# Optimization experiments

Measured on AMD Instinct MI355X. Metric: run time of the kernel, lower is better.

Reference implementation:

```python
import jax, jax.numpy as jnp
import numpy as np

B, S, D, H = 8, 1024, 512, 8
HD = D // H
EPS = 1e-5


def layer_norm(x, g, b):
    m = jnp.mean(x, axis=-1, keepdims=True)
    v = jnp.mean(jnp.square(x - m), axis=-1, keepdims=True)
    return (x - m) * jax.lax.rsqrt(v + EPS) * g + b


def mha(x, w_in, b_in, w_out, b_out):
    # x: [B,S,D]; w_in: [3D,D]; PyTorch MultiheadAttention math (no dropout, eval)
    b, s, d = x.shape
    qkv = x @ w_in.T + b_in                      # [B,S,3D]
    q, k, v = jnp.split(qkv, 3, axis=-1)
    q = q.reshape(b, s, H, HD)
    k = k.reshape(b, s, H, HD)
    v = v.reshape(b, s, H, HD)
    scores = jnp.einsum('bqhd,bkhd->bhqk', q, k) / np.sqrt(HD)
    a = jax.nn.softmax(scores, axis=-1)
    o = jnp.einsum('bhqk,bkhd->bqhd', a, v).reshape(b, s, d)
    return o @ w_out.T + b_out


def interp_linear(y, out_size):
    # y: [B,S_in,D]; torch F.interpolate(mode='linear', align_corners=False)
    s_in = y.shape[1]
    scale = s_in / out_size
    src = (jnp.arange(out_size, dtype=jnp.float32) + 0.5) * scale - 0.5
    src = jnp.clip(src, 0.0, s_in - 1.0)
    i0 = jnp.floor(src).astype(jnp.int32)
    i1 = jnp.minimum(i0 + 1, s_in - 1)
    w = (src - i0.astype(jnp.float32))[None, :, None]
    return y[:, i0, :] * (1.0 - w) + y[:, i1, :] * w


def setup_inputs() -> dict:
    key = jax.random.key(0)
    ks = jax.random.split(key, 16)
    sd = 0.02
    return {
        'x': jax.random.normal(ks[0], (B, S, D), jnp.float32),
        'w_in1': jax.random.normal(ks[1], (3 * D, D), jnp.float32) * sd,
        'b_in1': jnp.zeros((3 * D,), jnp.float32),
        'w_out1': jax.random.normal(ks[2], (D, D), jnp.float32) * sd,
        'b_out1': jnp.zeros((D,), jnp.float32),
        'w_in2': jax.random.normal(ks[3], (3 * D, D), jnp.float32) * sd,
        'b_in2': jnp.zeros((3 * D,), jnp.float32),
        'w_out2': jax.random.normal(ks[4], (D, D), jnp.float32) * sd,
        'b_out2': jnp.zeros((D,), jnp.float32),
        'g1': jnp.ones((D,), jnp.float32), 'beta1': jnp.zeros((D,), jnp.float32),
        'g2': jnp.ones((D,), jnp.float32), 'beta2': jnp.zeros((D,), jnp.float32),
        'g3': jnp.ones((D,), jnp.float32), 'beta3': jnp.zeros((D,), jnp.float32),
        'w_ff1': jax.random.normal(ks[5], (4 * D, D), jnp.float32) * sd,
        'b_ff1': jnp.zeros((4 * D,), jnp.float32),
        'w_ff2': jax.random.normal(ks[6], (D, 4 * D), jnp.float32) * sd,
        'b_ff2': jnp.zeros((D,), jnp.float32),
    }


def reference(x, w_in1, b_in1, w_out1, b_out1, w_in2, b_in2, w_out2, b_out2,
              g1, beta1, g2, beta2, g3, beta3, w_ff1, b_ff1, w_ff2, b_ff2):
    a1 = mha(x, w_in1, b_in1, w_out1, b_out1)
    x = layer_norm(x + a1, g1, beta1)
    # avg_pool1d kernel=2 stride=2 ceil_mode (S even -> exact halving)
    pooled = x.reshape(B, S // 2, 2, D).mean(axis=2)
    a2 = mha(pooled, w_in2, b_in2, w_out2, b_out2)
    up = interp_linear(a2, S)
    x = layer_norm(x + up, g2, beta2)
    h = jax.nn.gelu(x @ w_ff1.T + b_ff1, approximate=False)
    ff = h @ w_ff2.T + b_ff2
    return layer_norm(x + ff, g3, beta3)
```

## Files before the change

### kernel.cpp

```cpp
#include <hip/hip_runtime.h>
#include <hip/hip_bf16.h>
#include <math.h>

typedef __hip_bfloat16 bf16;
typedef __attribute__((ext_vector_type(8))) short short8;
typedef __attribute__((ext_vector_type(4))) short s4v;
typedef __attribute__((ext_vector_type(4))) float f32x4;

__device__ __forceinline__ float ldf(const float* p, size_t i) { return p[i]; }
__device__ __forceinline__ float ldf(const bf16*  p, size_t i) { return __bfloat162float(p[i]); }
__device__ __forceinline__ void  stf(float* p, size_t i, float v) { p[i] = v; }
__device__ __forceinline__ void  stf(bf16*  p, size_t i, float v) { p[i] = __float2bfloat16(v); }

__device__ __forceinline__ float ex2(float x) { return __builtin_amdgcn_exp2f(x); }

__device__ __forceinline__ void gl16(const void* gp, void* lp) {
    __builtin_amdgcn_global_load_lds(
        (const __attribute__((address_space(1))) void*)gp,
        (__attribute__((address_space(3))) void*)lp, 16, 0, 0);
}

__global__ __launch_bounds__(256) void cvt_kernel(
    const float* __restrict__ src, bf16* __restrict__ dst, int n)
{
    for (int i = blockIdx.x * 256 + threadIdx.x; i < n; i += gridDim.x * 256)
        dst[i] = __float2bfloat16(src[i]);
}

__global__ __launch_bounds__(256) void cvt_w(
    const float* __restrict__ s0, const float* __restrict__ s1,
    const float* __restrict__ s2, const float* __restrict__ s3,
    const float* __restrict__ s4, const float* __restrict__ s5,
    bf16* __restrict__ dst)
{
    int i = blockIdx.x * 256 + threadIdx.x;
    const float* s; int off;
    if      (i <  786432) { s = s0; off = 0; }
    else if (i < 1048576) { s = s1; off =  786432; }
    else if (i < 1835008) { s = s2; off = 1048576; }
    else if (i < 2097152) { s = s3; off = 1835008; }
    else if (i < 3145728) { s = s4; off = 2097152; }
    else                  { s = s5; off = 3145728; }
    dst[i] = __float2bfloat16(s[i - off]);
}

template <int EPI>
__global__ __launch_bounds__(256) void gemm_mfma(
    const bf16* __restrict__ A, const bf16* __restrict__ W,
    const float* __restrict__ bias, bf16* __restrict__ C,
    int M, int N, int K)
{
    __shared__ __align__(16) bf16 Asl[128 * 64];
    __shared__ __align__(16) bf16 Bsl[128 * 64];

    const int tid  = threadIdx.x;
    const int lane = tid & 63;
    const int wave = tid >> 6;
    const int wm   = wave >> 1;
    const int wn   = wave & 1;
    const int l15  = lane & 15;
    const int quad = lane >> 4;
    const int sr   = lane >> 3;
    const int sc   = (lane & 7) * 8;

    const int row0 = blockIdx.y * 128, col0 = blockIdx.x * 128;

    f32x4 acc[4][4] = {};

    for (int k0 = 0; k0 < K; k0 += 64) {
        __syncthreads();
        #pragma unroll
        for (int t = 0; t < 4; t++) {
            int r0 = wave * 32 + t * 8;
            int r  = r0 + sr;
            gl16(&A[(size_t)(row0 + r) * K + k0 + sc], &Asl[r0 * 64]);
            gl16(&W[(size_t)(col0 + r) * K + k0 + sc], &Bsl[r0 * 64]);
        }
        __syncthreads();

        #pragma unroll
        for (int ks = 0; ks < 64; ks += 32) {
            short8 af[4], bfr[4];
            #pragma unroll
            for (int mt = 0; mt < 4; mt++)
                af[mt] = *(const short8*)&Asl[(wm * 64 + mt * 16 + l15) * 64 + ks + quad * 8];
            #pragma unroll
            for (int nt = 0; nt < 4; nt++)
                bfr[nt] = *(const short8*)&Bsl[(wn * 64 + nt * 16 + l15) * 64 + ks + quad * 8];
            #pragma unroll
            for (int mt = 0; mt < 4; mt++)
                #pragma unroll
                for (int nt = 0; nt < 4; nt++)
                    acc[mt][nt] = __builtin_amdgcn_mfma_f32_16x16x32_bf16(
                        af[mt], bfr[nt], acc[mt][nt], 0, 0, 0);
        }
    }

    #pragma unroll
    for (int mt = 0; mt < 4; mt++) {
        int row = row0 + wm * 64 + mt * 16 + quad * 4;
        #pragma unroll
        for (int nt = 0; nt < 4; nt++) {
            int col = col0 + wn * 64 + nt * 16 + l15;
            float bv = bias[col];
            #pragma unroll
            for (int r = 0; r < 4; r++) {
                float v = acc[mt][nt][r] + bv;
                if (EPI == 1) v = 0.5f * v * (1.0f + erff(v * 0.70710678118654752f));
                C[(size_t)(row + r) * N + col] = __float2bfloat16(v);
            }
        }
    }
}

template <int NS>
__global__ __launch_bounds__(256) void flash_attn_mfma(
    const bf16* __restrict__ qkv, bf16* __restrict__ o, int S)
{
    __shared__ __align__(16) bf16 Ks[64 * 72];
    __shared__ __align__(16) bf16 Vt[64 * 68];
    __shared__ __align__(16) bf16 Pl[4][NS * 16 * 72];
    __shared__ float aX[4][NS * 16];

    const int tid = threadIdx.x;
    const int wave = tid >> 6, lane = tid & 63;
    const int l15 = lane & 15, quad = lane >> 4;
    const int q0 = blockIdx.x * (64 * NS), h = blockIdx.y, bb = blockIdx.z;
    const bf16* base = qkv + (size_t)bb * S * 1536 + h * 64;

    short8 qf[NS][2];
    #pragma unroll
    for (int s = 0; s < NS; s++) {
        size_t qoff = (size_t)(q0 + (wave * NS + s) * 16 + l15) * 1536;
        qf[s][0] = *(const short8*)&base[qoff + quad * 8];
        qf[s][1] = *(const short8*)&base[qoff + 32 + quad * 8];
    }

    f32x4 oacc[NS][4] = {};
    float mrow[NS], lrow[NS];
    #pragma unroll
    for (int s = 0; s < NS; s++) { mrow[s] = -3.0e38f; lrow[s] = 0.f; }

    const float CE = 0.18033688f;

    for (int k0 = 0; k0 < S; k0 += 64) {
        __syncthreads();

        #pragma unroll
        for (int t = 0; t < 2; t++) {
            int c = tid + 256 * t;
            int r = c >> 3, col = (c & 7) * 8;
            *(short8*)&Ks[r * 72 + col] =
                *(const short8*)&base[(size_t)(k0 + r) * 1536 + 512 + col];
        }
        #pragma unroll
        for (int i = 0; i < 8; i++) {
            int r = (wave * 8 + i) * 2;
            union { bf16 b[2]; unsigned u; } pk;
            pk.b[0] = base[(size_t)(k0 + r) * 1536 + 1024 + lane];
            pk.b[1] = base[(size_t)(k0 + r + 1) * 1536 + 1024 + lane];
            *(unsigned*)&Vt[lane * 68 + r] = pk.u;
        }
        __syncthreads();

        f32x4 st[NS][4] = {};
        #pragma unroll
        for (int mt = 0; mt < 4; mt++) {
            short8 kf0 = *(const short8*)&Ks[(mt * 16 + l15) * 72 + quad * 8];
            short8 kf1 = *(const short8*)&Ks[(mt * 16 + l15) * 72 + 32 + quad * 8];
            #pragma unroll
            for (int s = 0; s < NS; s++) {
                st[s][mt] = __builtin_amdgcn_mfma_f32_16x16x32_bf16(kf0, qf[s][0], st[s][mt], 0, 0, 0);
                st[s][mt] = __builtin_amdgcn_mfma_f32_16x16x32_bf16(kf1, qf[s][1], st[s][mt], 0, 0, 0);
            }
        }

        #pragma unroll
        for (int s = 0; s < NS; s++) {
            float cm = -3.0e38f;
            #pragma unroll
            for (int mt = 0; mt < 4; mt++)
                #pragma unroll
                for (int r = 0; r < 4; r++) cm = fmaxf(cm, st[s][mt][r]);
            cm = fmaxf(cm, __shfl_xor(cm, 16));
            cm = fmaxf(cm, __shfl_xor(cm, 32));
            float mn = fmaxf(mrow[s], cm);
            float alpha = ex2((mrow[s] - mn) * CE);
            mrow[s] = mn;
            float mb = mn * CE;
            float ps = 0.f;
            #pragma unroll
            for (int mt = 0; mt < 4; mt++) {
                s4v pw;
                #pragma unroll
                for (int r = 0; r < 4; r++) {
                    float p = ex2(st[s][mt][r] * CE - mb);
                    ps += p;
                    union { bf16 b; short h; } cv;
                    cv.b = __float2bfloat16(p);
                    pw[r] = cv.h;
                }
                *(s4v*)&Pl[wave][(s * 16 + l15) * 72 + mt * 16 + quad * 4] = pw;
            }
            ps += __shfl_xor(ps, 16);
            ps += __shfl_xor(ps, 32);
            lrow[s] = lrow[s] * alpha + ps;
            if (quad == 0) aX[wave][s * 16 + l15] = alpha;
        }

        #pragma unroll
        for (int s = 0; s < NS; s++) {
            float a4[4];
            #pragma unroll
            for (int r = 0; r < 4; r++) a4[r] = aX[wave][s * 16 + quad * 4 + r];
            #pragma unroll
            for (int nt = 0; nt < 4; nt++)
                #pragma unroll
                for (int r = 0; r < 4; r++) oacc[s][nt][r] *= a4[r];
        }

        #pragma unroll
        for (int kb = 0; kb < 2; kb++) {
            short8 pf[NS];
            #pragma unroll
            for (int s = 0; s < NS; s++)
                pf[s] = *(const short8*)&Pl[wave][(s * 16 + l15) * 72 + kb * 32 + quad * 8];
            #pragma unroll
            for (int nt = 0; nt < 4; nt++) {
                const bf16* vp = &Vt[(nt * 16 + l15) * 68 + kb * 32 + quad * 8];
                short8 vf;
                *(long*)&vf = *(const long*)vp;
                *((long*)&vf + 1) = *(const long*)(vp + 4);
                #pragma unroll
                for (int s = 0; s < NS; s++)
                    oacc[s][nt] = __builtin_amdgcn_mfma_f32_16x16x32_bf16(pf[s], vf, oacc[s][nt], 0, 0, 0);
            }
        }
    }

    #pragma unroll
    for (int s = 0; s < NS; s++)
        if (quad == 0) aX[wave][s * 16 + l15] = 1.0f / lrow[s];
    #pragma unroll
    for (int s = 0; s < NS; s++) {
        float iv[4];
        #pragma unroll
        for (int r = 0; r < 4; r++) iv[r] = aX[wave][s * 16 + quad * 4 + r];
        #pragma unroll
        for (int nt = 0; nt < 4; nt++)
            #pragma unroll
            for (int r = 0; r < 4; r++) {
                size_t row = (size_t)bb * S + q0 + (wave * NS + s) * 16 + quad * 4 + r;
                o[row * 512 + h * 64 + nt * 16 + l15] = __float2bfloat16(oacc[s][nt][r] * iv[r]);
            }
    }
}

template <typename AT, typename OT, bool INTERP>
__global__ __launch_bounds__(256) void ln_kernel(
    const AT* __restrict__ a, const bf16* __restrict__ bsrc,
    const float* __restrict__ g, const float* __restrict__ beta,
    OT* __restrict__ out)
{
    const int row = blockIdx.x;
    const int t = threadIdx.x;
    const size_t base = (size_t)row * 512;

    float a0 = ldf(a, base + t), a1 = ldf(a, base + t + 256);
    float b0, b1;
    if (INTERP) {
        int s = row & 1023, bb = row >> 10;
        float src = fminf(fmaxf((s + 0.5f) * 0.5f - 0.5f, 0.f), 511.f);
        int i0 = (int)src;
        int i1 = min(i0 + 1, 511);
        float w = src - (float)i0;
        size_t r0 = ((size_t)bb * 512 + i0) * 512;
        size_t r1 = ((size_t)bb * 512 + i1) * 512;
        b0 = __bfloat162float(bsrc[r0 + t]) * (1.f - w) + __bfloat162float(bsrc[r1 + t]) * w;
        b1 = __bfloat162float(bsrc[r0 + t + 256]) * (1.f - w) + __bfloat162float(bsrc[r1 + t + 256]) * w;
    } else {
        b0 = __bfloat162float(bsrc[base + t]);
        b1 = __bfloat162float(bsrc[base + t + 256]);
    }
    float v0 = a0 + b0, v1 = a1 + b1;

    __shared__ float red[4];
    const int lane = t & 63, wid = t >> 6;

    float sm = v0 + v1;
    #pragma unroll
    for (int off = 32; off > 0; off >>= 1) sm += __shfl_xor(sm, off);
    if (lane == 0) red[wid] = sm;
    __syncthreads();
    sm = red[0] + red[1] + red[2] + red[3];
    const float mean = sm * (1.0f / 512.0f);

    float d0 = v0 - mean, d1 = v1 - mean;
    float vv = d0 * d0 + d1 * d1;
    __syncthreads();
    #pragma unroll
    for (int off = 32; off > 0; off >>= 1) vv += __shfl_xor(vv, off);
    if (lane == 0) red[wid] = vv;
    __syncthreads();
    vv = red[0] + red[1] + red[2] + red[3];
    const float rstd = rsqrtf(vv * (1.0f / 512.0f) + 1e-5f);

    stf(out, base + t,       d0 * rstd * g[t]       + beta[t]);
    stf(out, base + t + 256, d1 * rstd * g[t + 256] + beta[t + 256]);
}

__global__ __launch_bounds__(256) void pool_kernel(
    const bf16* __restrict__ x, bf16* __restrict__ p)
{
    size_t i = (size_t)blockIdx.x * 256 + threadIdx.x;
    size_t d = i & 511;
    size_t rs = i >> 9;
    size_t b = rs >> 9, s = rs & 511;
    size_t r = (b * 1024 + 2 * s) * 512 + d;
    p[i] = __float2bfloat16(0.5f * (__bfloat162float(x[r]) + __bfloat162float(x[r + 512])));
}

extern "C" void kernel_launch(void* const* d_in, const int* in_sizes, int n_in,
                              void* d_out, int out_size, void* d_ws, size_t ws_size,
                              hipStream_t stream)
{
    const float* x      = (const float*)d_in[0];
    const float* w_in1  = (const float*)d_in[1];
    const float* b_in1  = (const float*)d_in[2];
    const float* w_out1 = (const float*)d_in[3];
    const float* b_out1 = (const float*)d_in[4];
    const float* w_in2  = (const float*)d_in[5];
    const float* b_in2  = (const float*)d_in[6];
    const float* w_out2 = (const float*)d_in[7];
    const float* b_out2 = (const float*)d_in[8];
    const float* g1     = (const float*)d_in[9];
    const float* be1    = (const float*)d_in[10];
    const float* g2     = (const float*)d_in[11];
    const float* be2    = (const float*)d_in[12];
    const float* g3     = (const float*)d_in[13];
    const float* be3    = (const float*)d_in[14];
    const float* w_ff1  = (const float*)d_in[15];
    const float* b_ff1  = (const float*)d_in[16];
    const float* w_ff2  = (const float*)d_in[17];
    const float* b_ff2  = (const float*)d_in[18];

    bf16* ws     = (bf16*)d_ws;
    bf16* xb     = ws + 0;
    bf16* wq1    = ws + 4194304;
    bf16* wo1    = ws + 4980736;
    bf16* wq2    = ws + 5242880;
    bf16* wo2    = ws + 6029312;
    bf16* wf1    = ws + 6291456;
    bf16* wf2    = ws + 7340032;
    bf16* qkv1   = ws + 8388608;
    bf16* o1     = ws + 20971520;
    bf16* a1     = ws + 25165824;
    bf16* x1     = ws + 29360128;
    bf16* pooled = ws + 33554432;
    bf16* qkv2   = ws + 35651584;
    bf16* o2     = ws + 41943040;
    bf16* a2     = ws + 44040192;
    bf16* x2     = ws + 46137344;
    bf16* h      = ws + 8388608;
    bf16* ff     = ws + 25165824;

    dim3 blk(256);

    cvt_kernel<<<4096, blk, 0, stream>>>(x, xb, 4194304);
    cvt_w<<<16384, blk, 0, stream>>>(w_in1, w_out1, w_in2, w_out2, w_ff1, w_ff2, wq1);

    gemm_mfma<0><<<dim3(12, 64), blk, 0, stream>>>(xb, wq1, b_in1, qkv1, 8192, 1536, 512);
    flash_attn_mfma<2><<<dim3(8, 8, 8), blk, 0, stream>>>(qkv1, o1, 1024);
    gemm_mfma<0><<<dim3(4, 64), blk, 0, stream>>>(o1, wo1, b_out1, a1, 8192, 512, 512);
    ln_kernel<float, bf16, false><<<8192, blk, 0, stream>>>(x, a1, g1, be1, x1);
    pool_kernel<<<8192, blk, 0, stream>>>(x1, pooled);
    gemm_mfma<0><<<dim3(12, 32), blk, 0, stream>>>(pooled, wq2, b_in2, qkv2, 4096, 1536, 512);
    flash_attn_mfma<1><<<dim3(8, 8, 8), blk, 0, stream>>>(qkv2, o2, 512);
    gemm_mfma<0><<<dim3(4, 32), blk, 0, stream>>>(o2, wo2, b_out2, a2, 4096, 512, 512);
    ln_kernel<bf16, bf16, true><<<8192, blk, 0, stream>>>(x1, a2, g2, be2, x2);
    gemm_mfma<1><<<dim3(16, 64), blk, 0, stream>>>(x2, wf1, b_ff1, h, 8192, 2048, 512);
    gemm_mfma<0><<<dim3(4, 64), blk, 0, stream>>>(h, wf2, b_ff2, ff, 8192, 512, 2048);
    ln_kernel<bf16, float, false><<<8192, blk, 0, stream>>>(x2, ff, g3, be3, (float*)d_out);
}
```

Baseline: 366.9 us.

## Double-buffer GEMM LDS tiles and XOR-swizzle to avoid bank conflicts

The bf16 MFMA GEMM now keeps two LDS buffers for the A and W tiles. The next K-tile's global-to-LDS loads are issued before the current tile is computed, so load latency can overlap MFMA work, and one barrier per iteration is removed. The 16-byte chunk positions within each row are also XOR-swizzled by the row index, both when stored and when read, to reduce LDS bank conflicts on the fragment loads. In exchange, LDS use doubles to 64KB per block, which may lower occupancy.

```diff
diff --git a/kernel.cpp b/kernel.cpp
--- a/kernel.cpp
+++ b/kernel.cpp
@@ -50,8 +50,8 @@
     const float* __restrict__ bias, bf16* __restrict__ C,
     int M, int N, int K)
 {
-    __shared__ __align__(16) bf16 Asl[128 * 64];
-    __shared__ __align__(16) bf16 Bsl[128 * 64];
+    __shared__ __align__(16) bf16 Asl[2][128 * 64];
+    __shared__ __align__(16) bf16 Bsl[2][128 * 64];
 
     const int tid  = threadIdx.x;
     const int lane = tid & 63;
@@ -61,32 +61,45 @@
     const int l15  = lane & 15;
     const int quad = lane >> 4;
     const int sr   = lane >> 3;
-    const int sc   = (lane & 7) * 8;
+    const int sc   = ((lane & 7) ^ sr) * 8;
 
     const int row0 = blockIdx.y * 128, col0 = blockIdx.x * 128;
 
     f32x4 acc[4][4] = {};
 
-    for (int k0 = 0; k0 < K; k0 += 64) {
+    const int nk = K >> 6;
+
+    #pragma unroll
+    for (int t = 0; t < 4; t++) {
+        int r0 = wave * 32 + t * 8;
+        gl16(&A[(size_t)(row0 + r0 + sr) * K + sc], &Asl[0][r0 * 64]);
+        gl16(&W[(size_t)(col0 + r0 + sr) * K + sc], &Bsl[0][r0 * 64]);
+    }
+
+    int cur = 0;
+    for (int i = 0; i < nk; i++) {
         __syncthreads();
-        #pragma unroll
-        for (int t = 0; t < 4; t++) {
-            int r0 = wave * 32 + t * 8;
-            int r  = r0 + sr;
-            gl16(&A[(size_t)(row0 + r) * K + k0 + sc], &Asl[r0 * 64]);
-            gl16(&W[(size_t)(col0 + r) * K + k0 + sc], &Bsl[r0 * 64]);
-        }
-        __syncthreads();
+        if (i + 1 < nk) {
+            int k1 = (i + 1) << 6;
+            #pragma unroll
+            for (int t = 0; t < 4; t++) {
+                int r0 = wave * 32 + t * 8;
+                gl16(&A[(size_t)(row0 + r0 + sr) * K + k1 + sc], &Asl[cur ^ 1][r0 * 64]);
+                gl16(&W[(size_t)(col0 + r0 + sr) * K + k1 + sc], &Bsl[cur ^ 1][r0 * 64]);
+            }
+        }
 
         #pragma unroll
         for (int ks = 0; ks < 64; ks += 32) {
             short8 af[4], bfr[4];
+            const int g0 = (ks >> 3) + quad;
+            const int col = (g0 ^ (l15 & 7)) * 8;
             #pragma unroll
             for (int mt = 0; mt < 4; mt++)
-                af[mt] = *(const short8*)&Asl[(wm * 64 + mt * 16 + l15) * 64 + ks + quad * 8];
+                af[mt] = *(const short8*)&Asl[cur][(wm * 64 + mt * 16 + l15) * 64 + col];
             #pragma unroll
             for (int nt = 0; nt < 4; nt++)
-                bfr[nt] = *(const short8*)&Bsl[(wn * 64 + nt * 16 + l15) * 64 + ks + quad * 8];
+                bfr[nt] = *(const short8*)&Bsl[cur][(wn * 64 + nt * 16 + l15) * 64 + col];
             #pragma unroll
             for (int mt = 0; mt < 4; mt++)
                 #pragma unroll
@@ -94,6 +107,7 @@
                     acc[mt][nt] = __builtin_amdgcn_mfma_f32_16x16x32_bf16(
                         af[mt], bfr[nt], acc[mt][nt], 0, 0, 0);
         }
+        cur ^= 1;
     }
 
     #pragma unroll
```

Measured after the change: 338.1 us. 1.09x faster.
